# Performance work log

Hardware: AMD Instinct MI355X
Metric: run time of the kernel (lower is better)

Reference implementation:

```python
import jax, jax.numpy as jnp
import numpy as np

D = 1024
EXPAND = 2
DI = EXPAND * D
K = 4           # d_conv
C = 64          # chunk_size
ALPHA = 0.9     # memory decay
B, S = 2, 8192
EPS = 1e-5


def setup_inputs() -> dict:
    key = jax.random.key(0)
    ks = jax.random.split(key, 10)
    s = 0.02
    return {
        "x": jax.random.normal(ks[0], (B, S, D), dtype=jnp.float32),
        "norm_w": jnp.ones((D,), dtype=jnp.float32),
        "w_up": jax.random.normal(ks[1], (D, DI), dtype=jnp.float32) * s,
        "w_gate": jax.random.normal(ks[2], (D, DI), dtype=jnp.float32) * s,
        "w_down": jax.random.normal(ks[3], (DI, D), dtype=jnp.float32) * s,
        "conv_w": jax.random.normal(ks[4], (K, 1, DI), dtype=jnp.float32) * s,  # WIO depthwise
        "conv_b": jnp.zeros((DI,), dtype=jnp.float32),
        "wq": jax.random.normal(ks[5], (D, D), dtype=jnp.float32) * s,
        "wk": jax.random.normal(ks[6], (D, D), dtype=jnp.float32) * s,
        "wv": jax.random.normal(ks[7], (D, D), dtype=jnp.float32) * s,
        "wo": jax.random.normal(ks[8], (D, D), dtype=jnp.float32) * s,
    }


def _rmsnorm(x, w):
    ms = jnp.mean(jnp.square(x.astype(jnp.float32)), axis=-1, keepdims=True)
    return (x * jax.lax.rsqrt(ms + EPS).astype(x.dtype)) * w


def _causal_depthwise_conv(u, conv_w, conv_b):
    # u: [B,S,DI]; depthwise causal conv over S, then SiLU
    y = jax.lax.conv_general_dilated(
        u, conv_w,
        window_strides=(1,), padding=[(K - 1, 0)],
        dimension_numbers=("NWC", "WIO", "NWC"),
        feature_group_count=DI)
    return jax.nn.silu(y + conv_b)


def _hebbian_memory(h, wq, wk, wv, wo):
    # chunked linear-attention style Hebbian memory
    b, s, d = h.shape
    n = s // C
    scale = d ** -0.5
    q = (h @ wq).reshape(b, n, C, d) * scale
    k = (h @ wk).reshape(b, n, C, d)
    v = (h @ wv).reshape(b, n, C, d)
    mask = jnp.tril(jnp.ones((C, C), dtype=h.dtype))  # inclusive causal within chunk

    def step(M, qkv):
        qc, kc, vc = qkv  # [b,C,d]
        inter = jnp.einsum("bcd,bde->bce", qc, M)
        attn = jnp.einsum("bcd,bed->bce", qc, kc) * mask
        intra = jnp.einsum("bce,bed->bcd", attn, vc)
        M_new = ALPHA * M + jnp.einsum("bcd,bce->bde", kc, vc)
        return M_new, inter + intra

    M0 = jnp.zeros((b, d, d), dtype=h.dtype)
    qkv = (jnp.swapaxes(q, 0, 1), jnp.swapaxes(k, 0, 1), jnp.swapaxes(v, 0, 1))
    _, o = jax.lax.scan(step, M0, qkv)        # [n,b,C,d]
    o = jnp.swapaxes(o, 0, 1).reshape(b, s, d)
    return o @ wo


def reference(x, norm_w, w_up, w_gate, w_down, conv_w, conv_b, wq, wk, wv, wo):
    normed = _rmsnorm(x, norm_w)
    val = _causal_depthwise_conv(normed @ w_up, conv_w, conv_b)   # [B,S,DI]
    gate = jax.nn.silu(normed @ w_gate)
    out = (gate * val) @ w_down                                   # [B,S,D]
    out = _hebbian_memory(out, wq, wk, wv, wo)
    return x + out
```

## Files before the change

kernel.cpp:

```cpp
#include <hip/hip_runtime.h>
#include <cstdint>
#include <cstddef>

#define SS 8192
#define DD 1024
#define DI2 2048
#define NR 16384

#define LOG2_09 (-0.152003093445050f)
#define LAMBDA16 0.185302018885184f

typedef __attribute__((ext_vector_type(4))) float f32x4;
typedef __attribute__((ext_vector_type(8))) __bf16 bf16x8;

union U16 { uint4 u; bf16x8 b; };

static __device__ __forceinline__ f32x4 MFMA(uint4 a, uint4 b, f32x4 c) {
  U16 ua, ub; ua.u = a; ub.u = b;
  return __builtin_amdgcn_mfma_f32_16x16x32_bf16(ua.b, ub.b, c, 0, 0, 0);
}

static __device__ __forceinline__ unsigned short f2bf(float f) {
  union { float f; unsigned u; } v; v.f = f;
  return (unsigned short)((v.u + 0x7FFFu + ((v.u >> 16) & 1u)) >> 16);
}
static __device__ __forceinline__ float bf2f(unsigned b) {
  union { unsigned u; float f; } v; v.u = b << 16; return v.f;
}
static __device__ __forceinline__ void unpack8(uint4 u, float* f) {
  f[0] = bf2f(u.x & 0xFFFFu); f[1] = bf2f(u.x >> 16);
  f[2] = bf2f(u.y & 0xFFFFu); f[3] = bf2f(u.y >> 16);
  f[4] = bf2f(u.z & 0xFFFFu); f[5] = bf2f(u.z >> 16);
  f[6] = bf2f(u.w & 0xFFFFu); f[7] = bf2f(u.w >> 16);
}

static __device__ __forceinline__ void glds16(const unsigned short* g, char* l) {
  __builtin_amdgcn_global_load_lds(
      (const __attribute__((address_space(1))) unsigned int*)g,
      (__attribute__((address_space(3))) unsigned int*)l, 16, 0, 0);
}

__global__ __launch_bounds__(256)
void transpose_cast(const float* __restrict__ in, unsigned short* __restrict__ out, int R, int Cc) {
  __shared__ float tile[32][33];
  const int r0 = blockIdx.y * 32, c0 = blockIdx.x * 32;
  const int tx = threadIdx.x, ty = threadIdx.y;
#pragma unroll
  for (int i = 0; i < 4; i++)
    tile[ty + i * 8][tx] = in[(size_t)(r0 + ty + i * 8) * Cc + c0 + tx];
  __syncthreads();
#pragma unroll
  for (int i = 0; i < 4; i++)
    out[(size_t)(c0 + ty + i * 8) * R + r0 + tx] = f2bf(tile[tx][ty + i * 8]);
}

__global__ __launch_bounds__(256)
void rmsnorm_kernel(const float* __restrict__ x, const float* __restrict__ w,
                    unsigned short* __restrict__ out) {
  const int row = blockIdx.x, t = threadIdx.x;
  const float4 v = ((const float4*)(x + (size_t)row * DD))[t];
  float ss = v.x * v.x + v.y * v.y + v.z * v.z + v.w * v.w;
  __shared__ float sred[256];
  sred[t] = ss;
  __syncthreads();
  for (int o = 128; o > 0; o >>= 1) {
    if (t < o) sred[t] += sred[t + o];
    __syncthreads();
  }
  const float rr = rsqrtf(sred[0] * (1.0f / (float)DD) + 1e-5f);
  const float4 wv = ((const float4*)w)[t];
  uint2 pk;
  pk.x = (unsigned)f2bf(v.x * rr * wv.x) | ((unsigned)f2bf(v.y * rr * wv.y) << 16);
  pk.y = (unsigned)f2bf(v.z * rr * wv.z) | ((unsigned)f2bf(v.w * rr * wv.w) << 16);
  *(uint2*)(out + (size_t)row * DD + t * 4) = pk;
}

enum { EP_BF16 = 0, EP_BF16_BOTH = 1, EP_BF16_T = 2, EP_F32_RES = 3, EP_STATE = 4,
       EP_CROSS = 5, EP_SCORE = 6, EP_PV = 7 };

template <int MODE>
__global__ __launch_bounds__(512, 2)
void gemm256(const unsigned short* __restrict__ A, const unsigned short* __restrict__ Bt,
             unsigned short* __restrict__ Cb, unsigned short* __restrict__ Ct,
             float* __restrict__ Cf, const float* __restrict__ resid,
             int M, int N, int kLen, int lda, int ldb, float scale) {
  __shared__ char sLds[131072];
  const int t = threadIdx.x, lane = t & 63, wid = t >> 6;
  const int wr = wid >> 2, wc = wid & 3;
  const int l15 = lane & 15, lh = lane >> 4;
  const int mblocks = M >> 8;
  int m0, n0;
  if constexpr (MODE == EP_SCORE) {
    const int p = (int)blockIdx.x;
    const int mt = (p >= 6) ? 3 : (p >= 3) ? 2 : (p >= 1) ? 1 : 0;
    const int nt = p - ((mt * (mt + 1)) >> 1);
    m0 = mt << 8; n0 = nt << 8;
  } else if ((mblocks & 7) == 0) {
    const int msl = mblocks >> 3;
    const int xcd = (int)blockIdx.x & 7, loc = (int)blockIdx.x >> 3;
    m0 = (xcd * msl + (loc % msl)) << 8;
    n0 = (loc / msl) << 8;
  } else {
    m0 = ((int)blockIdx.x % mblocks) << 8;
    n0 = ((int)blockIdx.x / mblocks) << 8;
  }
  int zb = 0, zg = 0;
  const unsigned short* Abase = A;
  const unsigned short* Bbase = Bt;
  if constexpr (MODE == EP_STATE || MODE == EP_CROSS || MODE == EP_SCORE || MODE == EP_PV) {
    const int gb = blockIdx.z;
    zb = gb >> 3; zg = gb & 7;
    if constexpr (MODE == EP_STATE) {
      Abase = A + (size_t)zb * DD * SS + (size_t)zg * 1024;
      Bbase = Bt + (size_t)zb * DD * SS + (size_t)zg * 1024;
    } else if constexpr (MODE == EP_CROSS) {
      Abase = A + ((size_t)zb * SS + (size_t)zg * 1024) * (size_t)lda;
      Bbase = Bt + ((size_t)blockIdx.z << 20);
    } else if constexpr (MODE == EP_SCORE) {
      Abase = A + ((size_t)zb * SS + (size_t)zg * 1024) * (size_t)lda;
      Bbase = Bt + ((size_t)zb * SS + (size_t)zg * 1024) * (size_t)ldb;
    } else {
      Abase = A + ((size_t)blockIdx.z << 20);
      Bbase = Bt + (size_t)zb * DD * SS + (size_t)zg * 1024;
    }
  }
  const int srow = wid * 16 + (lane >> 2);
  const int scol = ((lane & 3) << 3) ^ (((srow >> 1) & 3) << 3);
  const unsigned short* pA0 = Abase + (size_t)(m0 + srow) * lda + scol;
  const unsigned short* pA1 = pA0 + (size_t)128 * lda;
  const unsigned short* pB0 = Bbase + (size_t)(n0 + srow) * ldb + scol;
  const unsigned short* pB1 = pB0 + (size_t)128 * ldb;
  const int ldsW = wid * 1024;
  int offA[8], offB[4];
#pragma unroll
  for (int mf = 0; mf < 8; mf++) {
    const int r = wr * 128 + mf * 16 + l15;
    offA[mf] = r * 64 + ((lh * 16) ^ (((r >> 1) & 3) << 4));
  }
#pragma unroll
  for (int nf = 0; nf < 4; nf++) {
    const int r = wc * 64 + nf * 16 + l15;
    offB[nf] = r * 64 + ((lh * 16) ^ (((r >> 1) & 3) << 4));
  }
  int NT = kLen >> 5;
  if constexpr (MODE == EP_PV) NT = ((m0 >> 8) + 1) << 3;
#define BUFA(tt) (sLds + ((tt) & 3) * 32768)
#define BUFB(tt) (sLds + ((tt) & 3) * 32768 + 16384)
#define STAGEA(tt) do { const int _k = (tt) * 32; \
    glds16(pA0 + _k, BUFA(tt) + ldsW); \
    glds16(pA1 + _k, BUFA(tt) + 8192 + ldsW); } while (0)
#define STAGEB(tt) do { const int _k = (tt) * 32; \
    glds16(pB0 + _k, BUFB(tt) + ldsW); \
    glds16(pB1 + _k, BUFB(tt) + 8192 + ldsW); } while (0)
  STAGEA(0); STAGEB(0); STAGEA(1); STAGEB(1); STAGEA(2); STAGEB(2);
  asm volatile("s_waitcnt vmcnt(8)" ::: "memory");
  __builtin_amdgcn_s_barrier();
  f32x4 acc[8][4] = {};
  for (int kt = 0; kt < NT; ++kt) {
    const char* At  = BUFA(kt);
    const char* Bt_ = BUFB(kt);
    uint4 av[4], bv[4], av2[4];
#pragma unroll
    for (int i = 0; i < 4; i++) av[i] = *(const uint4*)(At + offA[i]);
#pragma unroll
    for (int i = 0; i < 4; i++) bv[i] = *(const uint4*)(Bt_ + offB[i]);
    if (kt + 3 < NT) STAGEA(kt + 3);
    __builtin_amdgcn_s_setprio(1);
#pragma unroll
    for (int mf = 0; mf < 4; mf++)
#pragma unroll
      for (int nf = 0; nf < 4; nf++)
        acc[mf][nf] = MFMA(av[mf], bv[nf], acc[mf][nf]);
    __builtin_amdgcn_s_setprio(0);
    __builtin_amdgcn_s_barrier();
#pragma unroll
    for (int i = 0; i < 4; i++) av2[i] = *(const uint4*)(At + offA[4 + i]);
    if (kt + 3 < NT) STAGEB(kt + 3);
    __builtin_amdgcn_s_setprio(1);
#pragma unroll
    for (int mf = 0; mf < 4; mf++)
#pragma unroll
      for (int nf = 0; nf < 4; nf++)
        acc[4 + mf][nf] = MFMA(av2[mf], bv[nf], acc[4 + mf][nf]);
    __builtin_amdgcn_s_setprio(0);
    if (kt < NT - 3)       { asm volatile("s_waitcnt vmcnt(8)" ::: "memory"); }
    else if (kt == NT - 3) { asm volatile("s_waitcnt vmcnt(4)" ::: "memory"); }
    else if (kt == NT - 2) { asm volatile("s_waitcnt vmcnt(0)" ::: "memory"); }
    __builtin_amdgcn_s_barrier();
  }
#undef STAGEA
#undef STAGEB
#undef BUFA
#undef BUFB
#pragma unroll
  for (int mf = 0; mf < 8; mf++) {
    const int r0 = m0 + wr * 128 + mf * 16 + lh * 4;
#pragma unroll
    for (int nf = 0; nf < 4; nf++) {
      const int c = n0 + wc * 64 + nf * 16 + l15;
      f32x4 v = acc[mf][nf] * scale;
      if constexpr (MODE == EP_F32_RES) {
#pragma unroll
        for (int jj = 0; jj < 4; jj++) {
          const size_t idx = (size_t)(r0 + jj) * N + c;
          Cf[idx] = v[jj] + resid[idx];
        }
      } else if constexpr (MODE == EP_STATE) {
        unsigned short* Tg = Cb + ((size_t)blockIdx.z << 20);
#pragma unroll
        for (int jj = 0; jj < 4; jj++)
          Tg[(size_t)(r0 + jj) * 1024 + c] = f2bf(v[jj]);
      } else if constexpr (MODE == EP_CROSS) {
        const float rs = exp2f((float)(r0 >> 6) * LOG2_09);
#pragma unroll
        for (int jj = 0; jj < 4; jj++) {
          const size_t idx = ((size_t)zb * SS + (size_t)zg * 1024 + r0 + jj) * DD + c;
          Cb[idx] = f2bf(bf2f(Cb[idx]) + v[jj] * rs);
        }
      } else if constexpr (MODE == EP_SCORE) {
        unsigned short* Sg = Cb + ((size_t)blockIdx.z << 20);
        const int qt = r0 >> 6;
        const int tb = c >> 6;
        float w;
        if (tb > qt)       w = 0.0f;
        else if (tb == qt) w = 1.0f;
        else               w = exp2f((float)(qt - 1 - tb) * LOG2_09);
#pragma unroll
        for (int jj = 0; jj < 4; jj++) {
          float val = v[jj] * w;
          if (tb == qt && (c & 63) > ((r0 + jj) & 63)) val = 0.0f;
          Sg[(size_t)(r0 + jj) * 1024 + c] = f2bf(val);
        }
      } else if constexpr (MODE == EP_PV) {
#pragma unroll
        for (int jj = 0; jj < 4; jj++)
          Cb[((size_t)zb * SS + (size_t)zg * 1024 + r0 + jj) * DD + c] = f2bf(v[jj]);
      } else {
        if constexpr (MODE == EP_BF16 || MODE == EP_BF16_BOTH) {
#pragma unroll
          for (int jj = 0; jj < 4; jj++)
            Cb[(size_t)(r0 + jj) * N + c] = f2bf(v[jj]);
        }
        if constexpr (MODE == EP_BF16_BOTH || MODE == EP_BF16_T) {
          const int bb = r0 >> 13, s0 = r0 & (SS - 1);
          float wt = 1.0f;
          if constexpr (MODE == EP_BF16_BOTH)
            wt = exp2f((float)(15 - ((s0 >> 6) & 15)) * LOG2_09);
          uint2 pk;
          pk.x = (unsigned)f2bf(v[0] * wt) | ((unsigned)f2bf(v[1] * wt) << 16);
          pk.y = (unsigned)f2bf(v[2] * wt) | ((unsigned)f2bf(v[3] * wt) << 16);
          *(uint2*)(Ct + ((size_t)bb * DD + c) * SS + s0) = pk;
        }
      }
    }
  }
}

__global__ __launch_bounds__(256)
void convgate_kernel(const unsigned short* __restrict__ ug, const float* __restrict__ cw,
                     const float* __restrict__ cb, unsigned short* __restrict__ hin) {
  const int r = blockIdx.x;
  const int c0 = threadIdx.x * 8;
  const int s = r & (SS - 1);
  float acc[8];
#pragma unroll
  for (int i = 0; i < 8; i++) acc[i] = cb[c0 + i];
  for (int tap = 0; tap < 4; tap++) {
    const int ds = s - 3 + tap;
    if (ds < 0) continue;
    uint4 uv = *(const uint4*)(ug + (size_t)(r - 3 + tap) * 4096 + c0);
    float u[8]; unpack8(uv, u);
#pragma unroll
    for (int i = 0; i < 8; i++) acc[i] += u[i] * cw[tap * DI2 + c0 + i];
  }
  uint4 gv = *(const uint4*)(ug + (size_t)r * 4096 + DI2 + c0);
  float gt[8]; unpack8(gv, gt);
  unsigned short o16[8];
#pragma unroll
  for (int i = 0; i < 8; i++) {
    const float val = acc[i] / (1.0f + __expf(-acc[i]));
    const float gg  = gt[i] / (1.0f + __expf(-gt[i]));
    o16[i] = f2bf(val * gg);
  }
  uint4 ov;
  ov.x = (unsigned)o16[0] | ((unsigned)o16[1] << 16);
  ov.y = (unsigned)o16[2] | ((unsigned)o16[3] << 16);
  ov.z = (unsigned)o16[4] | ((unsigned)o16[5] << 16);
  ov.w = (unsigned)o16[6] | ((unsigned)o16[7] << 16);
  *(uint4*)(hin + (size_t)r * DI2 + c0) = ov;
}

__global__ __launch_bounds__(256)
void prefix_kernel(unsigned short* __restrict__ Tb) {
  const int tid = blockIdx.x * 256 + threadIdx.x;
  const int b = tid >> 17, i = tid & 131071;
  unsigned short* p = Tb + (((size_t)b * 8) << 20) + (size_t)i * 8;
  float acc[8] = {};
  for (int g = 0; g < 8; g++) {
    unsigned short* pg = p + ((size_t)g << 20);
    uint4 tv = *(uint4*)pg;
    float tf_[8]; unpack8(tv, tf_);
    uint4 ov;
    ov.x = (unsigned)f2bf(acc[0]) | ((unsigned)f2bf(acc[1]) << 16);
    ov.y = (unsigned)f2bf(acc[2]) | ((unsigned)f2bf(acc[3]) << 16);
    ov.z = (unsigned)f2bf(acc[4]) | ((unsigned)f2bf(acc[5]) << 16);
    ov.w = (unsigned)f2bf(acc[6]) | ((unsigned)f2bf(acc[7]) << 16);
    *(uint4*)pg = ov;
#pragma unroll
    for (int e = 0; e < 8; e++) acc[e] = LAMBDA16 * acc[e] + tf_[e];
  }
}

extern "C" void kernel_launch(void* const* d_in, const int* in_sizes, int n_in,
                              void* d_out, int out_size, void* d_ws, size_t ws_size,
                              hipStream_t stream) {
  (void)in_sizes; (void)n_in; (void)out_size;
  const float* x      = (const float*)d_in[0];
  const float* norm_w = (const float*)d_in[1];
  const float* w_up   = (const float*)d_in[2];
  const float* w_gate = (const float*)d_in[3];
  const float* w_down = (const float*)d_in[4];
  const float* conv_w = (const float*)d_in[5];
  const float* conv_b = (const float*)d_in[6];
  const float* wq     = (const float*)d_in[7];
  const float* wk     = (const float*)d_in[8];
  const float* wv     = (const float*)d_in[9];
  const float* wo     = (const float*)d_in[10];
  float* out = (float*)d_out;

  const size_t MB = 1ull << 20;
  if (ws_size < 212 * MB) return;
  char* base = (char*)d_ws;
  unsigned short* ug     = (unsigned short*)(base + 0);
  unsigned short* hbuf   = (unsigned short*)(base + 0);
  unsigned short* Tbuf   = (unsigned short*)(base + 0);
  unsigned short* qbuf   = (unsigned short*)(base + 32 * MB);
  unsigned short* kbuf   = (unsigned short*)(base + 64 * MB);
  unsigned short* ktbuf  = (unsigned short*)(base + 96 * MB);
  unsigned short* sbuf   = (unsigned short*)(base + 96 * MB);
  unsigned short* normed = (unsigned short*)(base + 128 * MB);
  unsigned short* hin    = (unsigned short*)(base + 128 * MB);
  unsigned short* vtbuf  = (unsigned short*)(base + 128 * MB);
  unsigned short* obuf   = (unsigned short*)(base + 160 * MB);
  unsigned short* wugt   = (unsigned short*)(base + 192 * MB);
  unsigned short* wdt    = (unsigned short*)(base + 200 * MB);
  unsigned short* wqt    = (unsigned short*)(base + 204 * MB);
  unsigned short* wkt    = (unsigned short*)(base + 206 * MB);
  unsigned short* wvt    = (unsigned short*)(base + 208 * MB);
  unsigned short* wot    = (unsigned short*)(base + 210 * MB);

  dim3 tb(32, 8);
  transpose_cast<<<dim3(DI2 / 32, DD / 32), tb, 0, stream>>>(w_up,   wugt,                    DD,  DI2);
  transpose_cast<<<dim3(DI2 / 32, DD / 32), tb, 0, stream>>>(w_gate, wugt + (size_t)DI2 * DD, DD,  DI2);
  transpose_cast<<<dim3(DD / 32, DI2 / 32), tb, 0, stream>>>(w_down, wdt, DI2, DD);
  transpose_cast<<<dim3(DD / 32, DD / 32),  tb, 0, stream>>>(wq, wqt, DD, DD);
  transpose_cast<<<dim3(DD / 32, DD / 32),  tb, 0, stream>>>(wk, wkt, DD, DD);
  transpose_cast<<<dim3(DD / 32, DD / 32),  tb, 0, stream>>>(wv, wvt, DD, DD);
  transpose_cast<<<dim3(DD / 32, DD / 32),  tb, 0, stream>>>(wo, wot, DD, DD);

  rmsnorm_kernel<<<NR, 256, 0, stream>>>(x, norm_w, normed);

  gemm256<EP_BF16><<<dim3((NR / 256) * (4096 / 256)), 512, 0, stream>>>(
      normed, wugt, ug, nullptr, nullptr, nullptr, NR, 4096, DD, DD, DD, 1.0f);

  convgate_kernel<<<NR, 256, 0, stream>>>(ug, conv_w, conv_b, hin);

  gemm256<EP_BF16><<<dim3((NR / 256) * (DD / 256)), 512, 0, stream>>>(
      hin, wdt, hbuf, nullptr, nullptr, nullptr, NR, DD, DI2, DI2, DI2, 1.0f);

  gemm256<EP_BF16><<<dim3((NR / 256) * (DD / 256)), 512, 0, stream>>>(
      hbuf, wqt, qbuf, nullptr, nullptr, nullptr, NR, DD, DD, DD, DD, 0.03125f);
  gemm256<EP_BF16_BOTH><<<dim3((NR / 256) * (DD / 256)), 512, 0, stream>>>(
      hbuf, wkt, kbuf, ktbuf, nullptr, nullptr, NR, DD, DD, DD, DD, 1.0f);
  gemm256<EP_BF16_T><<<dim3((NR / 256) * (DD / 256)), 512, 0, stream>>>(
      hbuf, wvt, nullptr, vtbuf, nullptr, nullptr, NR, DD, DD, DD, DD, 1.0f);

  gemm256<EP_STATE><<<dim3(16, 1, 16), 512, 0, stream>>>(
      vtbuf, ktbuf, Tbuf, nullptr, nullptr, nullptr, 1024, 1024, 1024, SS, SS, 1.0f);
  gemm256<EP_SCORE><<<dim3(10, 1, 16), 512, 0, stream>>>(
      qbuf, kbuf, sbuf, nullptr, nullptr, nullptr, 1024, 1024, 1024, DD, DD, 1.0f);
  prefix_kernel<<<1024, 256, 0, stream>>>(Tbuf);
  gemm256<EP_PV><<<dim3(16, 1, 16), 512, 0, stream>>>(
      sbuf, vtbuf, obuf, nullptr, nullptr, nullptr, 1024, 1024, 1024, 1024, SS, 1.0f);
  gemm256<EP_CROSS><<<dim3(16, 1, 16), 512, 0, stream>>>(
      qbuf, Tbuf, obuf, nullptr, nullptr, nullptr, 1024, 1024, 1024, DD, 1024, 1.0f);

  gemm256<EP_F32_RES><<<dim3((NR / 256) * (DD / 256)), 512, 0, stream>>>(
      obuf, wot, nullptr, nullptr, out, x, NR, DD, DD, DD, DD, 1.0f);
}
```

Measured before the change: 697.3 us.

## Fuse Q/K/V projections into one GEMM and merge main-loop MFMA halves

Concatenates the transposed wq/wk/wv weights so the three projections run as a single N=3072 GEMM, with a new epilogue that routes each 1024-column section to the q, k/k-transposed-decayed, or v-transposed buffers. This removes two kernel launches and gives the grid more tiles. Separately, the GEMM main loop now loads all 8 A fragments at once, issues both A and B stages together, and drops the mid-iteration barrier. That raises register pressure and changes how LDS reads interleave with global-to-LDS prefetch in every GEMM.

```diff
diff --git a/kernel.cpp b/kernel.cpp
--- a/kernel.cpp
+++ b/kernel.cpp
@@ -76,7 +76,7 @@
 }
 
 enum { EP_BF16 = 0, EP_BF16_BOTH = 1, EP_BF16_T = 2, EP_F32_RES = 3, EP_STATE = 4,
-       EP_CROSS = 5, EP_SCORE = 6, EP_PV = 7 };
+       EP_CROSS = 5, EP_SCORE = 6, EP_PV = 7, EP_QKV = 8 };
 
 template <int MODE>
 __global__ __launch_bounds__(512, 2)
@@ -159,29 +159,18 @@
   for (int kt = 0; kt < NT; ++kt) {
     const char* At  = BUFA(kt);
     const char* Bt_ = BUFB(kt);
-    uint4 av[4], bv[4], av2[4];
-#pragma unroll
-    for (int i = 0; i < 4; i++) av[i] = *(const uint4*)(At + offA[i]);
+    uint4 av[8], bv[4];
+#pragma unroll
+    for (int i = 0; i < 8; i++) av[i] = *(const uint4*)(At + offA[i]);
 #pragma unroll
     for (int i = 0; i < 4; i++) bv[i] = *(const uint4*)(Bt_ + offB[i]);
-    if (kt + 3 < NT) STAGEA(kt + 3);
+    if (kt + 3 < NT) { STAGEA(kt + 3); STAGEB(kt + 3); }
     __builtin_amdgcn_s_setprio(1);
 #pragma unroll
-    for (int mf = 0; mf < 4; mf++)
+    for (int mf = 0; mf < 8; mf++)
 #pragma unroll
       for (int nf = 0; nf < 4; nf++)
         acc[mf][nf] = MFMA(av[mf], bv[nf], acc[mf][nf]);
-    __builtin_amdgcn_s_setprio(0);
-    __builtin_amdgcn_s_barrier();
-#pragma unroll
-    for (int i = 0; i < 4; i++) av2[i] = *(const uint4*)(At + offA[4 + i]);
-    if (kt + 3 < NT) STAGEB(kt + 3);
-    __builtin_amdgcn_s_setprio(1);
-#pragma unroll
-    for (int mf = 0; mf < 4; mf++)
-#pragma unroll
-      for (int nf = 0; nf < 4; nf++)
-        acc[4 + mf][nf] = MFMA(av2[mf], bv[nf], acc[4 + mf][nf]);
     __builtin_amdgcn_s_setprio(0);
     if (kt < NT - 3)       { asm volatile("s_waitcnt vmcnt(8)" ::: "memory"); }
     else if (kt == NT - 3) { asm volatile("s_waitcnt vmcnt(4)" ::: "memory"); }
@@ -235,6 +224,32 @@
 #pragma unroll
         for (int jj = 0; jj < 4; jj++)
           Cb[((size_t)zb * SS + (size_t)zg * 1024 + r0 + jj) * DD + c] = f2bf(v[jj]);
+      } else if constexpr (MODE == EP_QKV) {
+        unsigned short* qb  = Cb;
+        unsigned short* kb  = Ct;
+        unsigned short* ktb = (unsigned short*)Cf;
+        unsigned short* vtb = (unsigned short*)const_cast<float*>(resid);
+        const int sect = c >> 10, cc = c & 1023;
+        const int bb = r0 >> 13, s0 = r0 & (SS - 1);
+        if (sect == 0) {
+#pragma unroll
+          for (int jj = 0; jj < 4; jj++)
+            qb[(size_t)(r0 + jj) * DD + cc] = f2bf(v[jj] * 0.03125f);
+        } else if (sect == 1) {
+#pragma unroll
+          for (int jj = 0; jj < 4; jj++)
+            kb[(size_t)(r0 + jj) * DD + cc] = f2bf(v[jj]);
+          const float wt = exp2f((float)(15 - ((s0 >> 6) & 15)) * LOG2_09);
+          uint2 pk;
+          pk.x = (unsigned)f2bf(v[0] * wt) | ((unsigned)f2bf(v[1] * wt) << 16);
+          pk.y = (unsigned)f2bf(v[2] * wt) | ((unsigned)f2bf(v[3] * wt) << 16);
+          *(uint2*)(ktb + ((size_t)bb * DD + cc) * SS + s0) = pk;
+        } else {
+          uint2 pk;
+          pk.x = (unsigned)f2bf(v[0]) | ((unsigned)f2bf(v[1]) << 16);
+          pk.y = (unsigned)f2bf(v[2]) | ((unsigned)f2bf(v[3]) << 16);
+          *(uint2*)(vtb + ((size_t)bb * DD + cc) * SS + s0) = pk;
+        }
       } else {
         if constexpr (MODE == EP_BF16 || MODE == EP_BF16_BOTH) {
 #pragma unroll
@@ -344,18 +359,16 @@
   unsigned short* obuf   = (unsigned short*)(base + 160 * MB);
   unsigned short* wugt   = (unsigned short*)(base + 192 * MB);
   unsigned short* wdt    = (unsigned short*)(base + 200 * MB);
-  unsigned short* wqt    = (unsigned short*)(base + 204 * MB);
-  unsigned short* wkt    = (unsigned short*)(base + 206 * MB);
-  unsigned short* wvt    = (unsigned short*)(base + 208 * MB);
+  unsigned short* wqkvt  = (unsigned short*)(base + 204 * MB);
   unsigned short* wot    = (unsigned short*)(base + 210 * MB);
 
   dim3 tb(32, 8);
   transpose_cast<<<dim3(DI2 / 32, DD / 32), tb, 0, stream>>>(w_up,   wugt,                    DD,  DI2);
   transpose_cast<<<dim3(DI2 / 32, DD / 32), tb, 0, stream>>>(w_gate, wugt + (size_t)DI2 * DD, DD,  DI2);
   transpose_cast<<<dim3(DD / 32, DI2 / 32), tb, 0, stream>>>(w_down, wdt, DI2, DD);
-  transpose_cast<<<dim3(DD / 32, DD / 32),  tb, 0, stream>>>(wq, wqt, DD, DD);
-  transpose_cast<<<dim3(DD / 32, DD / 32),  tb, 0, stream>>>(wk, wkt, DD, DD);
-  transpose_cast<<<dim3(DD / 32, DD / 32),  tb, 0, stream>>>(wv, wvt, DD, DD);
+  transpose_cast<<<dim3(DD / 32, DD / 32),  tb, 0, stream>>>(wq, wqkvt,                          DD, DD);
+  transpose_cast<<<dim3(DD / 32, DD / 32),  tb, 0, stream>>>(wk, wqkvt + (size_t)DD * DD,       DD, DD);
+  transpose_cast<<<dim3(DD / 32, DD / 32),  tb, 0, stream>>>(wv, wqkvt + (size_t)2 * DD * DD,   DD, DD);
   transpose_cast<<<dim3(DD / 32, DD / 32),  tb, 0, stream>>>(wo, wot, DD, DD);
 
   rmsnorm_kernel<<<NR, 256, 0, stream>>>(x, norm_w, normed);
@@ -368,12 +381,9 @@
   gemm256<EP_BF16><<<dim3((NR / 256) * (DD / 256)), 512, 0, stream>>>(
       hin, wdt, hbuf, nullptr, nullptr, nullptr, NR, DD, DI2, DI2, DI2, 1.0f);
 
-  gemm256<EP_BF16><<<dim3((NR / 256) * (DD / 256)), 512, 0, stream>>>(
-      hbuf, wqt, qbuf, nullptr, nullptr, nullptr, NR, DD, DD, DD, DD, 0.03125f);
-  gemm256<EP_BF16_BOTH><<<dim3((NR / 256) * (DD / 256)), 512, 0, stream>>>(
-      hbuf, wkt, kbuf, ktbuf, nullptr, nullptr, NR, DD, DD, DD, DD, 1.0f);
-  gemm256<EP_BF16_T><<<dim3((NR / 256) * (DD / 256)), 512, 0, stream>>>(
-      hbuf, wvt, nullptr, vtbuf, nullptr, nullptr, NR, DD, DD, DD, DD, 1.0f);
+  gemm256<EP_QKV><<<dim3((NR / 256) * (3072 / 256)), 512, 0, stream>>>(
+      hbuf, wqkvt, qbuf, kbuf, (float*)ktbuf, (const float*)vtbuf,
+      NR, 3072, DD, DD, DD, 1.0f);
 
   gemm256<EP_STATE><<<dim3(16, 1, 16), 512, 0, stream>>>(
       vtbuf, ktbuf, Tbuf, nullptr, nullptr, nullptr, 1024, 1024, 1024, SS, SS, 1.0f);
```

New measurement: 669.1 us, median of 2. 1.04x faster.
